# Performance work log

Measured on AMD Instinct MI355X. Metric: run time of the kernel, lower is better.

## Reference

```python
import jax, jax.numpy as jnp
import numpy as np

N_NODES = 50000
N_EDGES = 800000
N_GRAPHS = 50
IN_DIM = 256
MID_DIM = 128
OUT_DIM = 256
EDGE_DIM = 128
EDGE_PROJ = 64


def _lin(key, din, dout):
    return jax.random.normal(key, (din, dout), dtype=jnp.float32) * 0.02


def setup_inputs() -> dict:
    key = jax.random.key(0)
    ks = jax.random.split(key, 32)
    x = jax.random.normal(ks[0], (N_NODES, IN_DIM), dtype=jnp.float32)
    edge_index = jax.random.randint(ks[1], (2, N_EDGES), 0, N_NODES, dtype=jnp.int32)
    edge_attr = jax.random.normal(ks[2], (N_EDGES, EDGE_DIM), dtype=jnp.float32)
    # 50 graphs of 1000 nodes each; node 0 of each graph is the master node
    batch = jnp.repeat(jnp.arange(N_GRAPHS, dtype=jnp.int32), N_NODES // N_GRAPHS)
    d = {
        "x": x, "edge_index": edge_index, "edge_attr": edge_attr, "batch": batch,
        "w_proj": _lin(ks[3], EDGE_DIM, EDGE_PROJ), "b_proj": jnp.zeros((EDGE_PROJ,), jnp.float32),
    }
    dims = [(IN_DIM, MID_DIM), (MID_DIM, MID_DIM), (MID_DIM, OUT_DIM)]
    ki = 4
    for i, (din, dout) in enumerate(dims, start=1):
        d[f"ws{i}"] = _lin(ks[ki], din, dout); ki += 1
        d[f"bs{i}"] = jnp.zeros((dout,), jnp.float32)
        d[f"wmx{i}"] = _lin(ks[ki], din, dout); ki += 1
        d[f"wme{i}"] = _lin(ks[ki], EDGE_PROJ, dout); ki += 1
        d[f"wes{i}"] = _lin(ks[ki], din, EDGE_PROJ); ki += 1
        d[f"wed{i}"] = _lin(ks[ki], din, EDGE_PROJ); ki += 1
        d[f"wee{i}"] = _lin(ks[ki], EDGE_PROJ, EDGE_PROJ); ki += 1
        d[f"be{i}"] = jnp.zeros((EDGE_PROJ,), jnp.float32)
    return d


def _conv(x, e, src, dst, ws, bs, wmx, wme, wes, wed, wee, be):
    # gather source/dest node feats, edge-conditioned message, scatter-add to dst
    xs = x[src]                                   # [E, din]
    xd = x[dst]                                   # [E, din]
    msg = xs @ wmx + e @ wme                      # [E, dout]
    agg = jax.ops.segment_sum(msg, dst, num_segments=N_NODES)  # [N, dout]
    x_out = x @ ws + bs + agg                     # [N, dout]
    e_out = xs @ wes + xd @ wed + e @ wee + be    # [E, edge_proj]
    return x_out, e_out


def reference(x, edge_index, edge_attr, batch, w_proj, b_proj,
              ws1, bs1, wmx1, wme1, wes1, wed1, wee1, be1,
              ws2, bs2, wmx2, wme2, wes2, wed2, wee2, be2,
              ws3, bs3, wmx3, wme3, wes3, wed3, wee3, be3):
    src, dst = edge_index[0], edge_index[1]
    e = edge_attr @ w_proj + b_proj               # project_edges
    x, e = _conv(x, e, src, dst, ws1, bs1, wmx1, wme1, wes1, wed1, wee1, be1)
    x, e = jax.nn.relu(x), jax.nn.relu(e)
    x, e = _conv(x, e, src, dst, ws2, bs2, wmx2, wme2, wes2, wed2, wee2, be2)
    x, e = jax.nn.relu(x), jax.nn.relu(e)
    x, e = _conv(x, e, src, dst, ws3, bs3, wmx3, wme3, wes3, wed3, wee3, be3)
    # global_master_pool: take first (master) node of each graph (batch is sorted)
    masters = jnp.searchsorted(batch, jnp.arange(N_GRAPHS, dtype=jnp.int32))
    return x[masters]                             # [n_graphs, out_dim]
```

## Files before the change

### kernel.cpp

```cpp
#include <hip/hip_runtime.h>

#define NN 50000
#define NE 800000
#define NG 50

typedef unsigned short u16;
typedef unsigned int u32;
typedef __attribute__((ext_vector_type(8))) short bf16x8;
typedef __attribute__((ext_vector_type(4))) float f32x4;

__device__ __forceinline__ float bf2f(u16 u){ u32 w = ((u32)u)<<16; float f; __builtin_memcpy(&f,&w,4); return f; }
__device__ __forceinline__ u16 f2bf(float f){ u32 w; __builtin_memcpy(&w,&f,4); u32 r = (w + 0x7fffu + ((w>>16)&1u)) >> 16; return (u16)r; }
__device__ __forceinline__ float ldf(const void* p, long long i, int bf){
  return bf ? bf2f(((const u16*)p)[i]) : ((const float*)p)[i];
}

__global__ void k_detect(const u32* __restrict__ words, int* __restrict__ flag){
  __shared__ int cnt;
  if (threadIdx.x==0) cnt = 0;
  __syncthreads();
  u32 w = words[threadIdx.x];
  int ex = (int)((w>>7)&0xffu);
  int hit = (w!=0u) && (ex>=100) && (ex<=150);
  atomicAdd(&cnt, hit);
  __syncthreads();
  if (threadIdx.x==0){ flag[0] = (cnt>128) ? 1 : 0; flag[1] = 0; }
}

struct InPtrs {
  const void *w_proj,*b_proj;
  const void *ws1,*bs1,*wmx1,*wme1,*wes1,*wed1,*wee1,*be1;
  const void *ws2,*bs2,*wmx2,*wme2,*wes2,*wed2,*wee2,*be2;
  const void *ws3,*bs3,*wmx3,*wme3,*wes3,*wed3,*wee3,*be3;
};
struct WPtrs {
  float *W1cat,*W2cat,*wprojf,*wme1f,*Wee1T,*wme2f,*wee2f,*wes2f,*wed2f,
        *wme3f,*wmx3f,*ws3f,*bproj,*bs1,*be1,*bs2,*be2,*bs3,
        *Wpe,*Wpm,*biaspe,*biaspm;
};

#define PREP_TOTAL 262848
__global__ void k_prep(InPtrs in, WPtrs w, const int* __restrict__ flagp){
  int bf = *flagp;
  for (long long i = (long long)blockIdx.x*256 + threadIdx.x; i < PREP_TOTAL; i += (long long)gridDim.x*256){
    long long r = i;
    if (r < 98304){ long long k=r/384, j=r%384; float v;
      if (j<128) v=ldf(in.wmx1,k*128+j,bf);
      else if (j<256) v=ldf(in.ws1,k*128+(j-128),bf);
      else if (j<320) v=ldf(in.wes1,k*64+(j-256),bf);
      else v=ldf(in.wed1,k*64+(j-320),bf);
      w.W1cat[r]=v; continue; } r -= 98304;
    if (r < 32768){ long long k=r/256, j=r%256; float v;
      if (j<128) v=ldf(in.wmx2,k*128+j,bf);
      else v=ldf(in.ws2,k*128+(j-128),bf);
      w.W2cat[r]=v; continue; } r -= 32768;
    if (r < 8192){  w.wprojf[r]=ldf(in.w_proj,r,bf); continue; } r -= 8192;
    if (r < 8192){  w.wme1f[r]=ldf(in.wme1,r,bf); continue;} r-=8192;
    if (r < 4096){  long long j=r/64,k=r%64; w.Wee1T[r]=ldf(in.wee1,k*64+j,bf);  continue;} r-=4096;
    if (r < 8192){  w.wme2f[r]=ldf(in.wme2,r,bf); continue;} r-=8192;
    if (r < 4096){  w.wee2f[r]=ldf(in.wee2,r,bf); continue;} r-=4096;
    if (r < 8192){  w.wes2f[r]=ldf(in.wes2,r,bf); continue;} r-=8192;
    if (r < 8192){  w.wed2f[r]=ldf(in.wed2,r,bf); continue;} r-=8192;
    if (r < 16384){ w.wme3f[r]=ldf(in.wme3,r,bf); continue;} r-=16384;
    if (r < 32768){ w.wmx3f[r]=ldf(in.wmx3,r,bf); continue;} r-=32768;
    if (r < 32768){ w.ws3f[r] =ldf(in.ws3,r,bf);  continue;} r-=32768;
    if (r < 64){  w.bproj[r]=ldf(in.b_proj,r,bf); continue;} r-=64;
    if (r < 128){ w.bs1[r]  =ldf(in.bs1,r,bf);   continue;} r-=128;
    if (r < 64){  w.be1[r]  =ldf(in.be1,r,bf);   continue;} r-=64;
    if (r < 128){ w.bs2[r]  =ldf(in.bs2,r,bf);   continue;} r-=128;
    if (r < 64){  w.be2[r]  =ldf(in.be2,r,bf);   continue;} r-=64;
    if (r < 256){ w.bs3[r]  =ldf(in.bs3,r,bf);   continue;}
  }
}

__global__ void k_prepmm(WPtrs w){
  const int tot = 8192 + 64 + 16384 + 128;
  for (int idx = blockIdx.x*256 + threadIdx.x; idx < tot; idx += gridDim.x*256){
    int r = idx;
    if (r < 8192){ int k=r>>6, j=r&63; float s=0.f;
      for (int m=0;m<64;++m) s += w.wprojf[k*64+m]*w.Wee1T[j*64+m];
      w.Wpe[r]=s; continue; } r -= 8192;
    if (r < 64){ float s=w.be1[r];
      for (int m=0;m<64;++m) s += w.bproj[m]*w.Wee1T[r*64+m];
      w.biaspe[r]=s; continue; } r -= 64;
    if (r < 16384){ int k=r>>7, j=r&127; float s=0.f;
      for (int m=0;m<64;++m) s += w.wprojf[k*64+m]*w.wme1f[m*128+j];
      w.Wpm[r]=s; continue; } r -= 16384;
    { float s=0.f; for (int m=0;m<64;++m) s += w.bproj[m]*w.wme1f[m*128+r];
      w.biaspm[r]=s; }
  }
}

__global__ void k_prepBG(const float* __restrict__ W, u16* __restrict__ Bf, int N, int total){
  int idx = blockIdx.x*256 + threadIdx.x;
  if (idx >= total) return;
  int i = idx & 7, l = (idx>>3) & 63, r = idx >> 9;
  int NT = N >> 4;
  int t = r % NT, ks = r / NT;
  int k = 32*ks + 8*(l>>4) + i;
  int col = 16*t + (l & 15);
  Bf[idx] = f2bf(W[(long long)k*N + col]);
}

__global__ void k_hist(const int* __restrict__ dstA, int* __restrict__ cnt){
  int e = blockIdx.x*256+threadIdx.x;
  atomicAdd(&cnt[dstA[e]], 1);
}
__global__ void k_scan1(const int* __restrict__ cnt, int* __restrict__ off, int* __restrict__ bsum){
  __shared__ int s[256];
  int b=blockIdx.x, t=threadIdx.x, i=b*256+t;
  int c = (i<NN)?cnt[i]:0;
  s[t]=c; __syncthreads();
  for (int o=1;o<256;o<<=1){ int u=(t>=o)?s[t-o]:0; __syncthreads(); s[t]+=u; __syncthreads(); }
  if (i<NN) off[i]=s[t]-c;
  if (t==255) bsum[b]=s[255];
}
__global__ void k_scan2(const int* __restrict__ bsum, int* __restrict__ bsumX, int nb){
  __shared__ int s[256];
  int t=threadIdx.x;
  int c = (t<nb)?bsum[t]:0;
  s[t]=c; __syncthreads();
  for (int o=1;o<256;o<<=1){ int u=(t>=o)?s[t-o]:0; __syncthreads(); s[t]+=u; __syncthreads(); }
  if (t<nb) bsumX[t]=s[t]-c;
}
__global__ void k_scan3(int* __restrict__ off, const int* __restrict__ bsumX, int* __restrict__ cur){
  int b=blockIdx.x, t=threadIdx.x, i=b*256+t;
  if (i<NN){ int v=off[i]+bsumX[b]; off[i]=v; cur[i]=v; }
  if (i==0) off[NN]=NE;
}
__global__ void k_scatter(const int* __restrict__ srcA, const int* __restrict__ dstA,
                          int* __restrict__ cur, int* __restrict__ perm,
                          int* __restrict__ srcP, int* __restrict__ dstP){
  int e = blockIdx.x*256+threadIdx.x;
  int d = dstA[e];
  int pos = atomicAdd(&cur[d],1);
  perm[pos]=e; srcP[pos]=srcA[e]; dstP[pos]=d;
}

__global__ __launch_bounds__(256) void k_gemm(const void* __restrict__ A, const int* __restrict__ aBfP,
                                              const float* __restrict__ B, float* __restrict__ C,
                                              int M, int K, int N){
  int aBf = *aBfP;
  __shared__ float As[16][68];
  __shared__ float Bs[16][68];
  int nb = N >> 6;
  int bx = blockIdx.x % nb, by = blockIdx.x / nb;
  int r0 = by<<6, c0 = bx<<6;
  int t = threadIdx.x, tx = t & 15, ty = t >> 4;
  float acc[4][4] = {{0.f}};
  for (int kk = 0; kk < K; kk += 16){
    int r = t >> 2, c4 = (t & 3) << 2;
    int row = r0 + r;
    float v0=0.f,v1=0.f,v2=0.f,v3=0.f;
    if (row < M){
      long long offa = (long long)row*K + kk + c4;
      if (aBf){ const u16* ap=(const u16*)A + offa; v0=bf2f(ap[0]); v1=bf2f(ap[1]); v2=bf2f(ap[2]); v3=bf2f(ap[3]); }
      else    { const float* ap=(const float*)A + offa; v0=ap[0]; v1=ap[1]; v2=ap[2]; v3=ap[3]; }
    }
    As[c4+0][r]=v0; As[c4+1][r]=v1; As[c4+2][r]=v2; As[c4+3][r]=v3;
    int rb = t >> 4, cb = (t & 15) << 2;
    const float* bp = B + (long long)(kk + rb)*N + c0 + cb;
    Bs[rb][cb+0]=bp[0]; Bs[rb][cb+1]=bp[1]; Bs[rb][cb+2]=bp[2]; Bs[rb][cb+3]=bp[3];
    __syncthreads();
    #pragma unroll
    for (int k=0;k<16;++k){
      float a0=As[k][(ty<<2)+0], a1=As[k][(ty<<2)+1], a2=As[k][(ty<<2)+2], a3=As[k][(ty<<2)+3];
      float b0=Bs[k][(tx<<2)+0], b1=Bs[k][(tx<<2)+1], b2=Bs[k][(tx<<2)+2], b3=Bs[k][(tx<<2)+3];
      acc[0][0]+=a0*b0; acc[0][1]+=a0*b1; acc[0][2]+=a0*b2; acc[0][3]+=a0*b3;
      acc[1][0]+=a1*b0; acc[1][1]+=a1*b1; acc[1][2]+=a1*b2; acc[1][3]+=a1*b3;
      acc[2][0]+=a2*b0; acc[2][1]+=a2*b1; acc[2][2]+=a2*b2; acc[2][3]+=a2*b3;
      acc[3][0]+=a3*b0; acc[3][1]+=a3*b1; acc[3][2]+=a3*b2; acc[3][3]+=a3*b3;
    }
    __syncthreads();
  }
  #pragma unroll
  for (int i=0;i<4;++i){
    int row = r0 + (ty<<2) + i;
    if (row < M){
      float* cp = C + (long long)row*N + c0 + (tx<<2);
      cp[0]=acc[i][0]; cp[1]=acc[i][1]; cp[2]=acc[i][2]; cp[3]=acc[i][3];
    }
  }
}

template<int K, int N>
__global__ __launch_bounds__(256) void k_gemmm(const void* __restrict__ A, const int* __restrict__ aBfP,
    const u16* __restrict__ Bf, float* __restrict__ C, int M){
  constexpr int NT = N/16, KS = K/32;
  int aBf = *aBfP;
  int wv = threadIdx.x >> 6, l = threadIdx.x & 63;
  int m = l & 15, kg = l >> 4;
  int row = blockIdx.x*64 + wv*16 + m;
  bf16x8 a[KS];
  if (row < M){
    if (aBf){
      const u16* ap = (const u16*)A + (long long)row*K;
      #pragma unroll
      for (int ks=0;ks<KS;++ks) a[ks] = *(const bf16x8*)(ap + ks*32 + kg*8);
    } else {
      const float* ap = (const float*)A + (long long)row*K;
      #pragma unroll
      for (int ks=0;ks<KS;++ks){
        float4 f0 = *(const float4*)(ap + ks*32 + kg*8);
        float4 f1 = *(const float4*)(ap + ks*32 + kg*8 + 4);
        bf16x8 v;
        v[0]=(short)f2bf(f0.x); v[1]=(short)f2bf(f0.y); v[2]=(short)f2bf(f0.z); v[3]=(short)f2bf(f0.w);
        v[4]=(short)f2bf(f1.x); v[5]=(short)f2bf(f1.y); v[6]=(short)f2bf(f1.z); v[7]=(short)f2bf(f1.w);
        a[ks]=v;
      }
    }
  } else {
    #pragma unroll
    for (int ks=0;ks<KS;++ks){
      bf16x8 z; 
      #pragma unroll
      for (int i=0;i<8;++i) z[i]=0;
      a[ks]=z;
    }
  }
  f32x4 acc[NT];
  #pragma unroll
  for (int t=0;t<NT;++t){ acc[t][0]=0.f; acc[t][1]=0.f; acc[t][2]=0.f; acc[t][3]=0.f; }
  #pragma unroll
  for (int t=0;t<NT;++t){
    #pragma unroll
    for (int ks=0;ks<KS;++ks){
      bf16x8 b = *(const bf16x8*)(Bf + ((size_t)(ks*NT + t)*64 + l)*8);
      acc[t] = __builtin_amdgcn_mfma_f32_16x16x32_bf16(b, a[ks], acc[t], 0, 0, 0);
    }
  }
  if (row < M){
    float* cp = C + (long long)row*N;
    #pragma unroll
    for (int t=0;t<NT;++t){
      int c0 = t*16 + kg*4;
      float4 o; o.x=acc[t][0]; o.y=acc[t][1]; o.z=acc[t][2]; o.w=acc[t][3];
      *(float4*)(cp + c0) = o;
    }
  }
}

__global__ __launch_bounds__(256) void k_projmm(const void* __restrict__ attr, const int* __restrict__ flagp,
    const int* __restrict__ perm,
    const u16* __restrict__ Bfrag, const float* __restrict__ biaspe, u16* __restrict__ P2){
  int abf = *flagp;
  int wv = threadIdx.x >> 6, l = threadIdx.x & 63;
  int m = l & 15, kg = l >> 4;
  long long pos = (long long)blockIdx.x*64 + wv*16 + m;
  long long e = perm[pos];
  bf16x8 a[4];
  if (abf){
    const u16* ap = (const u16*)attr + e*128;
    #pragma unroll
    for (int ks=0;ks<4;++ks) a[ks] = *(const bf16x8*)(ap + ks*32 + kg*8);
  } else {
    const float* ap = (const float*)attr + e*128;
    #pragma unroll
    for (int ks=0;ks<4;++ks){
      bf16x8 v;
      #pragma unroll
      for (int i=0;i<8;++i) v[i] = (short)f2bf(ap[ks*32 + kg*8 + i]);
      a[ks] = v;
    }
  }
  f32x4 acc[4];
  #pragma unroll
  for (int t4=0;t4<4;++t4){ acc[t4][0]=0.f; acc[t4][1]=0.f; acc[t4][2]=0.f; acc[t4][3]=0.f; }
  #pragma unroll
  for (int t4=0;t4<4;++t4){
    #pragma unroll
    for (int ks=0;ks<4;++ks){
      bf16x8 b = *(const bf16x8*)(Bfrag + (((ks<<2)|t4)*64 + l)*8);
      acc[t4] = __builtin_amdgcn_mfma_f32_16x16x32_bf16(b, a[ks], acc[t4], 0, 0, 0);
    }
  }
  u16* rp = P2 + pos*64;
  #pragma unroll
  for (int t4=0;t4<4;++t4){
    int col0 = t4*16 + kg*4;
    float4 bi = *(const float4*)(biaspe + col0);
    uint2 q;
    q.x = (u32)f2bf(acc[t4][0]+bi.x) | ((u32)f2bf(acc[t4][1]+bi.y)<<16);
    q.y = (u32)f2bf(acc[t4][2]+bi.z) | ((u32)f2bf(acc[t4][3]+bi.w)<<16);
    *(uint2*)(rp + col0) = q;
  }
}

__global__ __launch_bounds__(256) void k_agg(const int* __restrict__ perm, const int* __restrict__ srcP,
    const int* __restrict__ off, const float* __restrict__ nodeOut, int strideN,
    const void* __restrict__ attr, const int* __restrict__ flagp,
    const u16* __restrict__ P2, u16* __restrict__ e1m,
    float* __restrict__ aggN, float* __restrict__ aggA, float* __restrict__ aggE1, int mode){
  int abf = *flagp;
  int wv = threadIdx.x >> 6, lane = threadIdx.x & 63;
  int d = blockIdx.x*4 + wv;
  int a = off[d], b = off[d+1];
  int j2 = lane*2;
  float n0=0.f, n1=0.f;
  if (mode){
    float aA0=0.f, aA1=0.f, qe=0.f;
    float dD = nodeOut[(long long)d*strideN + 320 + lane];
    int isM = (d % 1000) == 0;
    u16* emp = e1m + (long long)(d/1000)*128*64;
    for (int pos=a; pos<b; ++pos){
      int src = srcP[pos];
      const float* nrow = nodeOut + (long long)src*strideN;
      float2 v = *(const float2*)(nrow + j2);
      int e = perm[pos];
      float t0,t1;
      if (abf){ ushort2 t2 = *(const ushort2*)((const u16*)attr + (long long)e*128 + j2); t0=bf2f(t2.x); t1=bf2f(t2.y); }
      else    { float2 t2 = *(const float2*)((const float*)attr + (long long)e*128 + j2); t0=t2.x; t1=t2.y; }
      float pw = bf2f(P2[(long long)pos*64 + lane]);
      float sv = nrow[256 + lane];
      float ev = fmaxf(pw + sv + dD, 0.f);
      n0 += v.x; n1 += v.y; aA0 += t0; aA1 += t1; qe += ev;
      if (isM && (pos-a) < 128) emp[(pos-a)*64 + lane] = f2bf(ev);
    }
    float2 w2; w2.x=aA0; w2.y=aA1;
    *(float2*)(aggA + (long long)d*128 + j2) = w2;
    aggE1[(long long)d*64 + lane] = qe;
  } else {
    int pos = a;
    for (; pos+1 < b; pos += 2){
      int s0 = srcP[pos], s1 = srcP[pos+1];
      float2 v0 = *(const float2*)(nodeOut + (long long)s0*strideN + j2);
      float2 v1 = *(const float2*)(nodeOut + (long long)s1*strideN + j2);
      n0 += v0.x + v1.x; n1 += v0.y + v1.y;
    }
    if (pos < b){
      float2 v0 = *(const float2*)(nodeOut + (long long)srcP[pos]*strideN + j2);
      n0 += v0.x; n1 += v0.y;
    }
  }
  float2 on; on.x=n0; on.y=n1;
  *(float2*)(aggN + (long long)d*128 + j2) = on;
}

__global__ void k_nodeupd(const float* __restrict__ nodeOut, int strideN,
                          const float* __restrict__ aggN, const float* __restrict__ aggEW,
                          const float* __restrict__ bs, const int* __restrict__ off,
                          const float* __restrict__ biasPM, int useDeg, float* __restrict__ xn){
  int i = blockIdx.x*256 + threadIdx.x;
  if (i >= NN*128) return;
  int n = i >> 7, j = i & 127;
  float v = nodeOut[(long long)n*strideN + 128 + j] + bs[j] + aggN[i] + aggEW[i];
  if (useDeg){ float deg = (float)(off[n+1]-off[n]); v += deg*biasPM[j]; }
  xn[i] = fmaxf(v, 0.f);
}

__global__ __launch_bounds__(256) void k_e2(const u16* __restrict__ e1m,
    const int* __restrict__ srcP, const int* __restrict__ off,
    const float* __restrict__ x1, const float* __restrict__ x2,
    WPtrs w, float* __restrict__ e2sum, float* __restrict__ x2sum){
  int g = blockIdx.x >> 6, i = blockIdx.x & 63;
  int master = g*1000;
  int s0 = off[master], deg = off[master+1]-s0;
  if (deg > 128) deg = 128;
  if (i >= deg) return;
  __shared__ float eL[64], x1s[128], x1m[128], part[4][64];
  int t = threadIdx.x;
  if (t < 128) x1m[t] = x1[(long long)master*128 + t];
  __syncthreads();
  for (int ii=i; ii<deg; ii+=64){
    int pos = s0+ii;
    int src = srcP[pos];
    if (t < 64) eL[t] = bf2f(e1m[((long long)g*128 + ii)*64 + t]);
    else if (t < 192) x1s[t-64] = x1[(long long)src*128 + (t-64)];
    __syncthreads();
    if (t < 128) atomicAdd(&x2sum[g*128+t], x2[(long long)src*128+t]);
    int j = t & 63, seg = t >> 6;
    float s = 0.f;
    int k0 = seg*80;
    #pragma unroll
    for (int q=0;q<80;++q){
      int kk = k0+q;
      float v; const float* wp;
      if (kk < 64){ v = eL[kk]; wp = w.wee2f + kk*64; }
      else if (kk < 192){ v = x1s[kk-64]; wp = w.wes2f + (kk-64)*64; }
      else { v = x1m[kk-192]; wp = w.wed2f + (kk-192)*64; }
      s += v * wp[j];
    }
    part[seg][j] = s;
    __syncthreads();
    if (t < 64){
      float v = part[0][t]+part[1][t]+part[2][t]+part[3][t] + w.be2[t];
      atomicAdd(&e2sum[g*64+t], fmaxf(v, 0.f));
    }
    __syncthreads();
  }
}

__global__ __launch_bounds__(256) void k_out(const float* __restrict__ x2,
    const float* __restrict__ e2sum, const float* __restrict__ x2sum,
    WPtrs w, void* __restrict__ out, const int* __restrict__ flagp){
  __shared__ float x2m[128], xs[128], es[64];
  int g = blockIdx.x, t = threadIdx.x;
  if (t < 128){ x2m[t] = x2[(long long)g*1000*128 + t]; xs[t] = x2sum[g*128+t]; }
  else if (t < 192) es[t-128] = e2sum[g*64 + (t-128)];
  __syncthreads();
  float o = w.bs3[t];
  #pragma unroll 4
  for (int k=0;k<128;++k) o += x2m[k]*w.ws3f[k*256+t] + xs[k]*w.wmx3f[k*256+t];
  #pragma unroll 4
  for (int k=0;k<64;++k)  o += es[k]*w.wme3f[k*256+t];
  if (*flagp) ((u16*)out)[g*256+t]=f2bf(o);
  else        ((float*)out)[g*256+t]=o;
}

extern "C" void kernel_launch(void* const* d_in, const int* in_sizes, int n_in,
                              void* d_out, int out_size, void* d_ws, size_t ws_size,
                              hipStream_t stream){
  const void* x0   = d_in[0];
  const int*  eidx = (const int*)d_in[1];
  const void* attr = d_in[2];
  InPtrs in;
  in.w_proj=d_in[4];  in.b_proj=d_in[5];
  in.ws1=d_in[6];  in.bs1=d_in[7];  in.wmx1=d_in[8];  in.wme1=d_in[9];  in.wes1=d_in[10]; in.wed1=d_in[11]; in.wee1=d_in[12]; in.be1=d_in[13];
  in.ws2=d_in[14]; in.bs2=d_in[15]; in.wmx2=d_in[16]; in.wme2=d_in[17]; in.wes2=d_in[18]; in.wed2=d_in[19]; in.wee2=d_in[20]; in.be2=d_in[21];
  in.ws3=d_in[22]; in.bs3=d_in[23]; in.wmx3=d_in[24]; in.wme3=d_in[25]; in.wes3=d_in[26]; in.wed3=d_in[27]; in.wee3=d_in[28]; in.be3=d_in[29];
  const int* srcA = eidx;
  const int* dstA = eidx + NE;

  char* p = (char*)d_ws;
  auto alloc = [&](size_t bytes){ void* r = (void*)p; p += (bytes + 255) & ~(size_t)255; return r; };
  int*   flag  = (int*)  alloc(256);
  float* wts   = (float*)alloc((size_t)PREP_TOTAL*4);
  float* wts2  = (float*)alloc((size_t)(8192+64+16384+128)*4);
  u16*   Bfrag = (u16*)  alloc((size_t)8192*2);
  u16*   W1f   = (u16*)  alloc((size_t)98304*2);
  u16*   W2f   = (u16*)  alloc((size_t)32768*2);
  int*   cnt   = (int*)  alloc((size_t)NN*4);
  int*   off   = (int*)  alloc((size_t)(NN+1)*4);
  int*   cur   = (int*)  alloc((size_t)NN*4);
  int*   bsum  = (int*)  alloc(256*4);
  int*   bsumX = (int*)  alloc(256*4);
  int*   perm  = (int*)  alloc((size_t)NE*4);
  int*   srcP  = (int*)  alloc((size_t)NE*4);
  int*   dstP  = (int*)  alloc((size_t)NE*4);
  u16*   P2    = (u16*)  alloc((size_t)NE*64*2);
  u16*   e1m   = (u16*)  alloc((size_t)NG*128*64*2);
  float* nodeOut=(float*)alloc((size_t)NN*384*4);
  float* aggN  = (float*)alloc((size_t)NN*128*4);
  float* aggA  = (float*)alloc((size_t)NN*128*4);
  float* aggE1 = (float*)alloc((size_t)NN*64*4);
  float* x1    = (float*)alloc((size_t)NN*128*4);
  float* x2    = (float*)alloc((size_t)NN*128*4);
  float* e2sum = (float*)alloc((size_t)NG*64*4);
  float* x2sum = (float*)alloc((size_t)NG*128*4);
  float* aggEW = (float*)P2;
  if ((size_t)(p - (char*)d_ws) > ws_size) return;

  WPtrs w; { float* q = wts;
    w.W1cat=q; q+=98304; w.W2cat=q; q+=32768; w.wprojf=q; q+=8192;
    w.wme1f=q; q+=8192; w.Wee1T=q; q+=4096; w.wme2f=q; q+=8192;
    w.wee2f=q; q+=4096; w.wes2f=q; q+=8192; w.wed2f=q; q+=8192;
    w.wme3f=q; q+=16384; w.wmx3f=q; q+=32768; w.ws3f=q; q+=32768;
    w.bproj=q; q+=64; w.bs1=q; q+=128; w.be1=q; q+=64;
    w.bs2=q; q+=128; w.be2=q; q+=64; w.bs3=q; q+=256; }
  { float* q = wts2;
    w.Wpe=q; q+=8192; w.biaspe=q; q+=64; w.Wpm=q; q+=16384; w.biaspm=q; q+=128; }

  const int GEMM_MB = (NN + 63)/64;
  const int SCAN_NB = (NN + 255)/256;

  k_detect<<<1,256,0,stream>>>((const u32*)attr, flag);
  k_prep<<<513,256,0,stream>>>(in, w, flag);
  k_prepmm<<<32,256,0,stream>>>(w);
  k_prepBG<<<32,256,0,stream>>>(w.Wpe, Bfrag, 64, 8192);
  k_prepBG<<<384,256,0,stream>>>(w.W1cat, W1f, 384, 98304);
  k_prepBG<<<128,256,0,stream>>>(w.W2cat, W2f, 256, 32768);

  hipMemsetAsync(cnt, 0, (size_t)NN*4, stream);
  k_hist<<<NE/256,256,0,stream>>>(dstA, cnt);
  k_scan1<<<SCAN_NB,256,0,stream>>>(cnt, off, bsum);
  k_scan2<<<1,256,0,stream>>>(bsum, bsumX, SCAN_NB);
  k_scan3<<<SCAN_NB,256,0,stream>>>(off, bsumX, cur);
  k_scatter<<<NE/256,256,0,stream>>>(srcA, dstA, cur, perm, srcP, dstP);
  hipMemsetAsync(e2sum, 0, (size_t)NG*64*4, stream);
  hipMemsetAsync(x2sum, 0, (size_t)NG*128*4, stream);

  k_gemmm<256,384><<<GEMM_MB,256,0,stream>>>(x0, flag, W1f, nodeOut, NN);
  k_projmm<<<NE/64,256,0,stream>>>(attr, flag, perm, Bfrag, w.biaspe, P2);
  k_agg<<<NN/4,256,0,stream>>>(perm, srcP, off, nodeOut, 384, attr, flag, P2, e1m,
                               aggN, aggA, aggE1, 1);
  k_gemm<<<GEMM_MB*2,256,0,stream>>>(aggA, flag+1, w.Wpm, aggEW, NN, 128, 128);
  k_nodeupd<<<(NN*128)/256,256,0,stream>>>(nodeOut, 384, aggN, aggEW, w.bs1, off, w.biaspm, 1, x1);

  k_gemmm<128,256><<<GEMM_MB,256,0,stream>>>(x1, flag+1, W2f, nodeOut, NN);
  k_agg<<<NN/4,256,0,stream>>>(perm, srcP, off, nodeOut, 256, attr, flag+1, P2, e1m,
                               aggN, aggA, aggE1, 0);
  k_gemm<<<GEMM_MB*2,256,0,stream>>>(aggE1, flag+1, w.wme2f, aggEW, NN, 64, 128);
  k_nodeupd<<<(NN*128)/256,256,0,stream>>>(nodeOut, 256, aggN, aggEW, w.bs2, off, w.biaspm, 0, x2);

  k_e2<<<NG*64,256,0,stream>>>(e1m, srcP, off, x1, x2, w, e2sum, x2sum);
  k_out<<<NG,256,0,stream>>>(x2, e2sum, x2sum, w, d_out, flag);
}
```

Before: 1.374 ms.

## Precompute projected edges in projmm and aggregate before weight GEMMs via MFMA

The edge projection E0 = attr@w_proj+b_proj is now computed alongside P2 in the MFMA projection kernel and stored as bf16 per edge. The layer-1 aggregation then sums the 64-wide E0 instead of re-reading 128-wide raw edge attributes through perm. Layer 2 aggregates x1 directly and applies [wmx2;wme2] after aggregation with an MFMA GEMM of K=192. The old scalar fp32 GEMM kernel is replaced by the MFMA kernel. This cuts gather bandwidth and GEMM cost, but adds an extra 100MB bf16 E0 write and some bf16 rounding.

```diff
diff --git a/kernel.cpp b/kernel.cpp
--- a/kernel.cpp
+++ b/kernel.cpp
@@ -36,10 +36,10 @@
 struct WPtrs {
   float *W1cat,*W2cat,*wprojf,*wme1f,*Wee1T,*wme2f,*wee2f,*wes2f,*wed2f,
         *wme3f,*wmx3f,*ws3f,*bproj,*bs1,*be1,*bs2,*be2,*bs3,
-        *Wpe,*Wpm,*biaspe,*biaspm;
+        *wm2cat,*ws2f,*Wpe,*biaspe;
 };
 
-#define PREP_TOTAL 262848
+#define PREP_TOTAL 303808
 __global__ void k_prep(InPtrs in, WPtrs w, const int* __restrict__ flagp){
   int bf = *flagp;
   for (long long i = (long long)blockIdx.x*256 + threadIdx.x; i < PREP_TOTAL; i += (long long)gridDim.x*256){
@@ -69,25 +69,25 @@
     if (r < 64){  w.be1[r]  =ldf(in.be1,r,bf);   continue;} r-=64;
     if (r < 128){ w.bs2[r]  =ldf(in.bs2,r,bf);   continue;} r-=128;
     if (r < 64){  w.be2[r]  =ldf(in.be2,r,bf);   continue;} r-=64;
-    if (r < 256){ w.bs3[r]  =ldf(in.bs3,r,bf);   continue;}
+    if (r < 256){ w.bs3[r]  =ldf(in.bs3,r,bf);   continue;} r-=256;
+    if (r < 24576){ long long k=r>>7, j=r&127; float v;
+      if (k<128) v=ldf(in.wmx2,k*128+j,bf);
+      else v=ldf(in.wme2,(k-128)*128+j,bf);
+      w.wm2cat[r]=v; continue;} r-=24576;
+    if (r < 16384){ w.ws2f[r]=ldf(in.ws2,r,bf); continue;}
   }
 }
 
 __global__ void k_prepmm(WPtrs w){
-  const int tot = 8192 + 64 + 16384 + 128;
+  const int tot = 8192 + 64;
   for (int idx = blockIdx.x*256 + threadIdx.x; idx < tot; idx += gridDim.x*256){
     int r = idx;
     if (r < 8192){ int k=r>>6, j=r&63; float s=0.f;
       for (int m=0;m<64;++m) s += w.wprojf[k*64+m]*w.Wee1T[j*64+m];
       w.Wpe[r]=s; continue; } r -= 8192;
-    if (r < 64){ float s=w.be1[r];
+    { float s=w.be1[r];
       for (int m=0;m<64;++m) s += w.bproj[m]*w.Wee1T[r*64+m];
-      w.biaspe[r]=s; continue; } r -= 64;
-    if (r < 16384){ int k=r>>7, j=r&127; float s=0.f;
-      for (int m=0;m<64;++m) s += w.wprojf[k*64+m]*w.wme1f[m*128+j];
-      w.Wpm[r]=s; continue; } r -= 16384;
-    { float s=0.f; for (int m=0;m<64;++m) s += w.bproj[m]*w.wme1f[m*128+r];
-      w.biaspm[r]=s; }
+      w.biaspe[r]=s; }
   }
 }
 
@@ -135,52 +135,6 @@
   int d = dstA[e];
   int pos = atomicAdd(&cur[d],1);
   perm[pos]=e; srcP[pos]=srcA[e]; dstP[pos]=d;
-}
-
-__global__ __launch_bounds__(256) void k_gemm(const void* __restrict__ A, const int* __restrict__ aBfP,
-                                              const float* __restrict__ B, float* __restrict__ C,
-                                              int M, int K, int N){
-  int aBf = *aBfP;
-  __shared__ float As[16][68];
-  __shared__ float Bs[16][68];
-  int nb = N >> 6;
-  int bx = blockIdx.x % nb, by = blockIdx.x / nb;
-  int r0 = by<<6, c0 = bx<<6;
-  int t = threadIdx.x, tx = t & 15, ty = t >> 4;
-  float acc[4][4] = {{0.f}};
-  for (int kk = 0; kk < K; kk += 16){
-    int r = t >> 2, c4 = (t & 3) << 2;
-    int row = r0 + r;
-    float v0=0.f,v1=0.f,v2=0.f,v3=0.f;
-    if (row < M){
-      long long offa = (long long)row*K + kk + c4;
-      if (aBf){ const u16* ap=(const u16*)A + offa; v0=bf2f(ap[0]); v1=bf2f(ap[1]); v2=bf2f(ap[2]); v3=bf2f(ap[3]); }
-      else    { const float* ap=(const float*)A + offa; v0=ap[0]; v1=ap[1]; v2=ap[2]; v3=ap[3]; }
-    }
-    As[c4+0][r]=v0; As[c4+1][r]=v1; As[c4+2][r]=v2; As[c4+3][r]=v3;
-    int rb = t >> 4, cb = (t & 15) << 2;
-    const float* bp = B + (long long)(kk + rb)*N + c0 + cb;
-    Bs[rb][cb+0]=bp[0]; Bs[rb][cb+1]=bp[1]; Bs[rb][cb+2]=bp[2]; Bs[rb][cb+3]=bp[3];
-    __syncthreads();
-    #pragma unroll
-    for (int k=0;k<16;++k){
-      float a0=As[k][(ty<<2)+0], a1=As[k][(ty<<2)+1], a2=As[k][(ty<<2)+2], a3=As[k][(ty<<2)+3];
-      float b0=Bs[k][(tx<<2)+0], b1=Bs[k][(tx<<2)+1], b2=Bs[k][(tx<<2)+2], b3=Bs[k][(tx<<2)+3];
-      acc[0][0]+=a0*b0; acc[0][1]+=a0*b1; acc[0][2]+=a0*b2; acc[0][3]+=a0*b3;
-      acc[1][0]+=a1*b0; acc[1][1]+=a1*b1; acc[1][2]+=a1*b2; acc[1][3]+=a1*b3;
-      acc[2][0]+=a2*b0; acc[2][1]+=a2*b1; acc[2][2]+=a2*b2; acc[2][3]+=a2*b3;
-      acc[3][0]+=a3*b0; acc[3][1]+=a3*b1; acc[3][2]+=a3*b2; acc[3][3]+=a3*b3;
-    }
-    __syncthreads();
-  }
-  #pragma unroll
-  for (int i=0;i<4;++i){
-    int row = r0 + (ty<<2) + i;
-    if (row < M){
-      float* cp = C + (long long)row*N + c0 + (tx<<2);
-      cp[0]=acc[i][0]; cp[1]=acc[i][1]; cp[2]=acc[i][2]; cp[3]=acc[i][3];
-    }
-  }
 }
 
 template<int K, int N>
@@ -212,7 +166,7 @@
   } else {
     #pragma unroll
     for (int ks=0;ks<KS;++ks){
-      bf16x8 z; 
+      bf16x8 z;
       #pragma unroll
       for (int i=0;i<8;++i) z[i]=0;
       a[ks]=z;
@@ -242,7 +196,9 @@
 
 __global__ __launch_bounds__(256) void k_projmm(const void* __restrict__ attr, const int* __restrict__ flagp,
     const int* __restrict__ perm,
-    const u16* __restrict__ Bfrag, const float* __restrict__ biaspe, u16* __restrict__ P2){
+    const u16* __restrict__ Bfrag, const float* __restrict__ biaspe,
+    const u16* __restrict__ WprojF, const float* __restrict__ bproj,
+    u16* __restrict__ P2, u16* __restrict__ E0){
   int abf = *flagp;
   int wv = threadIdx.x >> 6, l = threadIdx.x & 63;
   int m = l & 15, kg = l >> 4;
@@ -263,88 +219,95 @@
       a[ks] = v;
     }
   }
-  f32x4 acc[4];
-  #pragma unroll
-  for (int t4=0;t4<4;++t4){ acc[t4][0]=0.f; acc[t4][1]=0.f; acc[t4][2]=0.f; acc[t4][3]=0.f; }
+  f32x4 accP[4], accE[4];
   #pragma unroll
   for (int t4=0;t4<4;++t4){
+    accP[t4][0]=0.f; accP[t4][1]=0.f; accP[t4][2]=0.f; accP[t4][3]=0.f;
+    accE[t4][0]=0.f; accE[t4][1]=0.f; accE[t4][2]=0.f; accE[t4][3]=0.f;
+  }
+  #pragma unroll
+  for (int t4=0;t4<4;++t4){
     #pragma unroll
     for (int ks=0;ks<4;++ks){
-      bf16x8 b = *(const bf16x8*)(Bfrag + (((ks<<2)|t4)*64 + l)*8);
-      acc[t4] = __builtin_amdgcn_mfma_f32_16x16x32_bf16(b, a[ks], acc[t4], 0, 0, 0);
+      bf16x8 bP = *(const bf16x8*)(Bfrag  + (((ks<<2)|t4)*64 + l)*8);
+      bf16x8 bE = *(const bf16x8*)(WprojF + (((ks<<2)|t4)*64 + l)*8);
+      accP[t4] = __builtin_amdgcn_mfma_f32_16x16x32_bf16(bP, a[ks], accP[t4], 0, 0, 0);
+      accE[t4] = __builtin_amdgcn_mfma_f32_16x16x32_bf16(bE, a[ks], accE[t4], 0, 0, 0);
     }
   }
   u16* rp = P2 + pos*64;
+  u16* ep = E0 + pos*64;
   #pragma unroll
   for (int t4=0;t4<4;++t4){
     int col0 = t4*16 + kg*4;
     float4 bi = *(const float4*)(biaspe + col0);
+    float4 bj = *(const float4*)(bproj + col0);
     uint2 q;
-    q.x = (u32)f2bf(acc[t4][0]+bi.x) | ((u32)f2bf(acc[t4][1]+bi.y)<<16);
-    q.y = (u32)f2bf(acc[t4][2]+bi.z) | ((u32)f2bf(acc[t4][3]+bi.w)<<16);
+    q.x = (u32)f2bf(accP[t4][0]+bi.x) | ((u32)f2bf(accP[t4][1]+bi.y)<<16);
+    q.y = (u32)f2bf(accP[t4][2]+bi.z) | ((u32)f2bf(accP[t4][3]+bi.w)<<16);
     *(uint2*)(rp + col0) = q;
-  }
-}
-
-__global__ __launch_bounds__(256) void k_agg(const int* __restrict__ perm, const int* __restrict__ srcP,
-    const int* __restrict__ off, const float* __restrict__ nodeOut, int strideN,
-    const void* __restrict__ attr, const int* __restrict__ flagp,
-    const u16* __restrict__ P2, u16* __restrict__ e1m,
-    float* __restrict__ aggN, float* __restrict__ aggA, float* __restrict__ aggE1, int mode){
-  int abf = *flagp;
+    uint2 r2;
+    r2.x = (u32)f2bf(accE[t4][0]+bj.x) | ((u32)f2bf(accE[t4][1]+bj.y)<<16);
+    r2.y = (u32)f2bf(accE[t4][2]+bj.z) | ((u32)f2bf(accE[t4][3]+bj.w)<<16);
+    *(uint2*)(ep + col0) = r2;
+  }
+}
+
+__global__ __launch_bounds__(256) void k_agg(const int* __restrict__ srcP, const int* __restrict__ off,
+    const float* __restrict__ nodeOut, const float* __restrict__ x1,
+    const u16* __restrict__ P2, const u16* __restrict__ E0, u16* __restrict__ e1m,
+    float* __restrict__ aggN, float* __restrict__ aggE0, float* __restrict__ agg2, int mode){
   int wv = threadIdx.x >> 6, lane = threadIdx.x & 63;
   int d = blockIdx.x*4 + wv;
   int a = off[d], b = off[d+1];
   int j2 = lane*2;
-  float n0=0.f, n1=0.f;
   if (mode){
-    float aA0=0.f, aA1=0.f, qe=0.f;
-    float dD = nodeOut[(long long)d*strideN + 320 + lane];
+    float n0=0.f, n1=0.f, qe=0.f, q0=0.f;
+    float dD = nodeOut[(long long)d*384 + 320 + lane];
     int isM = (d % 1000) == 0;
     u16* emp = e1m + (long long)(d/1000)*128*64;
     for (int pos=a; pos<b; ++pos){
       int src = srcP[pos];
-      const float* nrow = nodeOut + (long long)src*strideN;
+      const float* nrow = nodeOut + (long long)src*384;
       float2 v = *(const float2*)(nrow + j2);
-      int e = perm[pos];
-      float t0,t1;
-      if (abf){ ushort2 t2 = *(const ushort2*)((const u16*)attr + (long long)e*128 + j2); t0=bf2f(t2.x); t1=bf2f(t2.y); }
-      else    { float2 t2 = *(const float2*)((const float*)attr + (long long)e*128 + j2); t0=t2.x; t1=t2.y; }
+      float sv = nrow[256 + lane];
       float pw = bf2f(P2[(long long)pos*64 + lane]);
-      float sv = nrow[256 + lane];
+      float e0v = bf2f(E0[(long long)pos*64 + lane]);
       float ev = fmaxf(pw + sv + dD, 0.f);
-      n0 += v.x; n1 += v.y; aA0 += t0; aA1 += t1; qe += ev;
+      n0 += v.x; n1 += v.y; qe += ev; q0 += e0v;
       if (isM && (pos-a) < 128) emp[(pos-a)*64 + lane] = f2bf(ev);
     }
-    float2 w2; w2.x=aA0; w2.y=aA1;
-    *(float2*)(aggA + (long long)d*128 + j2) = w2;
-    aggE1[(long long)d*64 + lane] = qe;
+    float2 on; on.x=n0; on.y=n1;
+    *(float2*)(aggN + (long long)d*128 + j2) = on;
+    aggE0[(long long)d*64 + lane] = q0;
+    agg2[(long long)d*192 + 128 + lane] = qe;
   } else {
+    float n0=0.f, n1=0.f;
     int pos = a;
     for (; pos+1 < b; pos += 2){
       int s0 = srcP[pos], s1 = srcP[pos+1];
-      float2 v0 = *(const float2*)(nodeOut + (long long)s0*strideN + j2);
-      float2 v1 = *(const float2*)(nodeOut + (long long)s1*strideN + j2);
+      float2 v0 = *(const float2*)(x1 + (long long)s0*128 + j2);
+      float2 v1 = *(const float2*)(x1 + (long long)s1*128 + j2);
       n0 += v0.x + v1.x; n1 += v0.y + v1.y;
     }
     if (pos < b){
-      float2 v0 = *(const float2*)(nodeOut + (long long)srcP[pos]*strideN + j2);
+      float2 v0 = *(const float2*)(x1 + (long long)srcP[pos]*128 + j2);
       n0 += v0.x; n1 += v0.y;
     }
-  }
-  float2 on; on.x=n0; on.y=n1;
-  *(float2*)(aggN + (long long)d*128 + j2) = on;
-}
-
-__global__ void k_nodeupd(const float* __restrict__ nodeOut, int strideN,
-                          const float* __restrict__ aggN, const float* __restrict__ aggEW,
-                          const float* __restrict__ bs, const int* __restrict__ off,
-                          const float* __restrict__ biasPM, int useDeg, float* __restrict__ xn){
+    float2 on; on.x=n0; on.y=n1;
+    *(float2*)(agg2 + (long long)d*192 + j2) = on;
+  }
+}
+
+__global__ void k_nodeupd(const float* __restrict__ base, int strideN, int colOff,
+                          const float* __restrict__ aggN, int useAggN,
+                          const float* __restrict__ aggEW,
+                          const float* __restrict__ bs, float* __restrict__ xn){
   int i = blockIdx.x*256 + threadIdx.x;
   if (i >= NN*128) return;
   int n = i >> 7, j = i & 127;
-  float v = nodeOut[(long long)n*strideN + 128 + j] + bs[j] + aggN[i] + aggEW[i];
-  if (useDeg){ float deg = (float)(off[n+1]-off[n]); v += deg*biasPM[j]; }
+  float v = base[(long long)n*strideN + colOff + j] + bs[j] + aggEW[i];
+  if (useAggN) v += aggN[i];
   xn[i] = fmaxf(v, 0.f);
 }
 
@@ -425,10 +388,13 @@
   auto alloc = [&](size_t bytes){ void* r = (void*)p; p += (bytes + 255) & ~(size_t)255; return r; };
   int*   flag  = (int*)  alloc(256);
   float* wts   = (float*)alloc((size_t)PREP_TOTAL*4);
-  float* wts2  = (float*)alloc((size_t)(8192+64+16384+128)*4);
+  float* wts2  = (float*)alloc((size_t)(8192+64)*4);
   u16*   Bfrag = (u16*)  alloc((size_t)8192*2);
+  u16*   WprojF= (u16*)  alloc((size_t)8192*2);
   u16*   W1f   = (u16*)  alloc((size_t)98304*2);
-  u16*   W2f   = (u16*)  alloc((size_t)32768*2);
+  u16*   Wme1F = (u16*)  alloc((size_t)8192*2);
+  u16*   Wm2F  = (u16*)  alloc((size_t)24576*2);
+  u16*   Ws2F  = (u16*)  alloc((size_t)16384*2);
   int*   cnt   = (int*)  alloc((size_t)NN*4);
   int*   off   = (int*)  alloc((size_t)(NN+1)*4);
   int*   cur   = (int*)  alloc((size_t)NN*4);
@@ -438,11 +404,12 @@
   int*   srcP  = (int*)  alloc((size_t)NE*4);
   int*   dstP  = (int*)  alloc((size_t)NE*4);
   u16*   P2    = (u16*)  alloc((size_t)NE*64*2);
+  u16*   E0    = (u16*)  alloc((size_t)NE*64*2);
   u16*   e1m   = (u16*)  alloc((size_t)NG*128*64*2);
   float* nodeOut=(float*)alloc((size_t)NN*384*4);
   float* aggN  = (float*)alloc((size_t)NN*128*4);
-  float* aggA  = (float*)alloc((size_t)NN*128*4);
-  float* aggE1 = (float*)alloc((size_t)NN*64*4);
+  float* aggE0 = (float*)alloc((size_t)NN*64*4);
+  float* agg2  = (float*)alloc((size_t)NN*192*4);
   float* x1    = (float*)alloc((size_t)NN*128*4);
   float* x2    = (float*)alloc((size_t)NN*128*4);
   float* e2sum = (float*)alloc((size_t)NG*64*4);
@@ -456,19 +423,23 @@
     w.wee2f=q; q+=4096; w.wes2f=q; q+=8192; w.wed2f=q; q+=8192;
     w.wme3f=q; q+=16384; w.wmx3f=q; q+=32768; w.ws3f=q; q+=32768;
     w.bproj=q; q+=64; w.bs1=q; q+=128; w.be1=q; q+=64;
-    w.bs2=q; q+=128; w.be2=q; q+=64; w.bs3=q; q+=256; }
+    w.bs2=q; q+=128; w.be2=q; q+=64; w.bs3=q; q+=256;
+    w.wm2cat=q; q+=24576; w.ws2f=q; q+=16384; }
   { float* q = wts2;
-    w.Wpe=q; q+=8192; w.biaspe=q; q+=64; w.Wpm=q; q+=16384; w.biaspm=q; q+=128; }
+    w.Wpe=q; q+=8192; w.biaspe=q; q+=64; }
 
   const int GEMM_MB = (NN + 63)/64;
   const int SCAN_NB = (NN + 255)/256;
 
   k_detect<<<1,256,0,stream>>>((const u32*)attr, flag);
   k_prep<<<513,256,0,stream>>>(in, w, flag);
-  k_prepmm<<<32,256,0,stream>>>(w);
+  k_prepmm<<<33,256,0,stream>>>(w);
   k_prepBG<<<32,256,0,stream>>>(w.Wpe, Bfrag, 64, 8192);
+  k_prepBG<<<32,256,0,stream>>>(w.wprojf, WprojF, 64, 8192);
   k_prepBG<<<384,256,0,stream>>>(w.W1cat, W1f, 384, 98304);
-  k_prepBG<<<128,256,0,stream>>>(w.W2cat, W2f, 256, 32768);
+  k_prepBG<<<32,256,0,stream>>>(w.wme1f, Wme1F, 128, 8192);
+  k_prepBG<<<96,256,0,stream>>>(w.wm2cat, Wm2F, 128, 24576);
+  k_prepBG<<<64,256,0,stream>>>(w.ws2f, Ws2F, 128, 16384);
 
   hipMemsetAsync(cnt, 0, (size_t)NN*4, stream);
   k_hist<<<NE/256,256,0,stream>>>(dstA, cnt);
@@ -480,17 +451,15 @@
   hipMemsetAsync(x2sum, 0, (size_t)NG*128*4, stream);
 
   k_gemmm<256,384><<<GEMM_MB,256,0,stream>>>(x0, flag, W1f, nodeOut, NN);
-  k_projmm<<<NE/64,256,0,stream>>>(attr, flag, perm, Bfrag, w.biaspe, P2);
-  k_agg<<<NN/4,256,0,stream>>>(perm, srcP, off, nodeOut, 384, attr, flag, P2, e1m,
-                               aggN, aggA, aggE1, 1);
-  k_gemm<<<GEMM_MB*2,256,0,stream>>>(aggA, flag+1, w.Wpm, aggEW, NN, 128, 128);
-  k_nodeupd<<<(NN*128)/256,256,0,stream>>>(nodeOut, 384, aggN, aggEW, w.bs1, off, w.biaspm, 1, x1);
-
-  k_gemmm<128,256><<<GEMM_MB,256,0,stream>>>(x1, flag+1, W2f, nodeOut, NN);
-  k_agg<<<NN/4,256,0,stream>>>(perm, srcP, off, nodeOut, 256, attr, flag+1, P2, e1m,
-                               aggN, aggA, aggE1, 0);
-  k_gemm<<<GEMM_MB*2,256,0,stream>>>(aggE1, flag+1, w.wme2f, aggEW, NN, 64, 128);
-  k_nodeupd<<<(NN*128)/256,256,0,stream>>>(nodeOut, 256, aggN, aggEW, w.bs2, off, w.biaspm, 0, x2);
+  k_projmm<<<NE/64,256,0,stream>>>(attr, flag, perm, Bfrag, w.biaspe, WprojF, w.bproj, P2, E0);
+  k_agg<<<NN/4,256,0,stream>>>(srcP, off, nodeOut, x1, P2, E0, e1m, aggN, aggE0, agg2, 1);
+  k_gemmm<64,128><<<GEMM_MB,256,0,stream>>>(aggE0, flag+1, Wme1F, aggEW, NN);
+  k_nodeupd<<<(NN*128)/256,256,0,stream>>>(nodeOut, 384, 128, aggN, 1, aggEW, w.bs1, x1);
+
+  k_gemmm<128,128><<<GEMM_MB,256,0,stream>>>(x1, flag+1, Ws2F, nodeOut, NN);
+  k_agg<<<NN/4,256,0,stream>>>(srcP, off, nodeOut, x1, P2, E0, e1m, aggN, aggE0, agg2, 0);
+  k_gemmm<192,128><<<GEMM_MB,256,0,stream>>>(agg2, flag+1, Wm2F, aggEW, NN);
+  k_nodeupd<<<(NN*128)/256,256,0,stream>>>(nodeOut, 128, 0, aggN, 0, aggEW, w.bs2, x2);
 
   k_e2<<<NG*64,256,0,stream>>>(e1m, srcP, off, x1, x2, w, e2sum, x2sum);
   k_out<<<NG,256,0,stream>>>(x2, e2sum, x2sum, w, d_out, flag);
```

New measurement: 1.310 ms. 1.05x faster.
